# Kernel optimization log

Measured on AMD Instinct MI355X. Metric: run time of the kernel, lower is better.

The kernel has to match this reference:

```python
import jax, jax.numpy as jnp
import numpy as np

# Repo globals / config
VOCAB_SIZE = 14
TOK_DIM = 8
POS_DIM = 8
D_MODEL = TOK_DIM + POS_DIM  # 16
MAX_SEQ_LEN = 2048
N_HEADS = 2
HEAD_DIM = 3
ATTN_DIM = N_HEADS * HEAD_DIM  # 6
FFN_DIM = 3
B, T = 16, 2048
EPS = 1e-5


def _ln(x, w, b):
    m = jnp.mean(x, axis=-1, keepdims=True)
    v = jnp.var(x, axis=-1, keepdims=True)
    return (x - m) * jax.lax.rsqrt(v + EPS) * w + b


def setup_inputs() -> dict:
    key = jax.random.key(0)
    ks = jax.random.split(key, 20)
    g = lambda k, shape: (jax.random.normal(k, shape, jnp.float32) * 0.1)
    return {
        "idx": jax.random.randint(ks[0], (B, T), 0, VOCAB_SIZE),
        "tok_emb": g(ks[1], (VOCAB_SIZE, TOK_DIM)),
        "pos_enc": g(ks[2], (MAX_SEQ_LEN, POS_DIM)),
        "Wq": g(ks[3], (ATTN_DIM, POS_DIM)),
        "Wk": g(ks[4], (ATTN_DIM, POS_DIM)),
        "Wv": g(ks[5], (ATTN_DIM, TOK_DIM)),
        "Wo": g(ks[6], (D_MODEL, ATTN_DIM)),
        "ln1_w": jnp.ones((D_MODEL,), jnp.float32),
        "ln1_b": jnp.zeros((D_MODEL,), jnp.float32),
        "ln2_w": jnp.ones((D_MODEL,), jnp.float32),
        "ln2_b": jnp.zeros((D_MODEL,), jnp.float32),
        "lnf_w": jnp.ones((D_MODEL,), jnp.float32),
        "lnf_b": jnp.zeros((D_MODEL,), jnp.float32),
        "W1": g(ks[7], (FFN_DIM, D_MODEL)),
        "b1": jnp.zeros((FFN_DIM,), jnp.float32),
        "W2": g(ks[8], (D_MODEL, FFN_DIM)),
        "b2": jnp.zeros((D_MODEL,), jnp.float32),
        "Wh": g(ks[9], (TOK_DIM, D_MODEL)),
    }


def reference(idx, tok_emb, pos_enc, Wq, Wk, Wv, Wo,
              ln1_w, ln1_b, ln2_w, ln2_b, lnf_w, lnf_b,
              W1, b1, W2, b2, Wh):
    Bq, Tq = idx.shape
    tok = tok_emb[idx]                                  # [B,T,TOK_DIM]
    pos = jnp.broadcast_to(pos_enc[:Tq][None], (Bq, Tq, POS_DIM))
    x = jnp.concatenate([tok, pos], axis=-1)            # [B,T,D_MODEL]
    h = _ln(x, ln1_w, ln1_b)
    x_tok = h[..., :TOK_DIM]
    x_pos = h[..., TOK_DIM:]
    # projections (torch Linear: y = x @ W.T)
    q = (x_pos @ Wq.T).reshape(Bq, Tq, N_HEADS, HEAD_DIM).transpose(0, 2, 1, 3)
    k = (x_pos @ Wk.T).reshape(Bq, Tq, N_HEADS, HEAD_DIM).transpose(0, 2, 1, 3)
    v = (x_tok @ Wv.T).reshape(Bq, Tq, N_HEADS, HEAD_DIM).transpose(0, 2, 1, 3)
    scores = jnp.einsum('bhqd,bhkd->bhqk', q, k) / jnp.sqrt(jnp.float32(HEAD_DIM))
    mask = jnp.tril(jnp.ones((Tq, Tq), dtype=bool))
    scores = jnp.where(mask[None, None], scores, -jnp.inf)
    attn = jax.nn.softmax(scores, axis=-1)
    out = jnp.einsum('bhqk,bhkd->bhqd', attn, v)
    out = out.transpose(0, 2, 1, 3).reshape(Bq, Tq, ATTN_DIM)
    x = x + out @ Wo.T
    h2 = _ln(x, ln2_w, ln2_b)
    x = x + (jax.nn.gelu(h2 @ W1.T + b1, approximate=False) @ W2.T + b2)
    x = _ln(x, lnf_w, lnf_b)
    return (x @ Wh.T) @ tok_emb.T                       # tied head -> [B,T,VOCAB]
```

## Files before the change

kernel.cpp:

```cpp
#include <hip/hip_runtime.h>
#include <hip/hip_fp16.h>
#include <math.h>

#define BB    16
#define TT    2048
#define VOCAB 14
#define TOKD  8
#define POSD  8
#define DM    16
#define NH    2
#define HD    3
#define AD    6
#define FFND  3

#define NTOK  (BB*TT)
#define BH    (BB*NH)
#define TPB   36
#define NTILE (BH*TPB)

struct P {
    const int*   idx;
    const float* tok_emb;
    const float* pos_enc;
    const float* Wq;
    const float* Wk;
    const float* Wv;
    const float* Wo;
    const float* ln1w;
    const float* ln1b;
    const float* ln2w;
    const float* ln2b;
    const float* lnfw;
    const float* lnfb;
    const float* W1;
    const float* b1;
    const float* W2;
    const float* b2;
    const float* Wh;
    float*       out;
    float4*      qbuf;
    uint4*       kvh;
    float4*      pbuf;
};

__global__ __launch_bounds__(256) void prep_kernel(P p) {
    int gid = blockIdx.x * 256 + threadIdx.x;
    if (gid >= NTOK) return;
    int t = gid & (TT - 1);
    int b = gid >> 11;

    float x[DM];
    int tok = p.idx[gid];
    #pragma unroll
    for (int j = 0; j < TOKD; ++j) x[j]        = p.tok_emb[tok * TOKD + j];
    #pragma unroll
    for (int j = 0; j < POSD; ++j) x[TOKD + j] = p.pos_enc[t * POSD + j];

    float m = 0.f;
    #pragma unroll
    for (int j = 0; j < DM; ++j) m += x[j];
    m *= (1.f / DM);
    float v = 0.f;
    #pragma unroll
    for (int j = 0; j < DM; ++j) { float d = x[j] - m; v += d * d; }
    v *= (1.f / DM);
    float rs = rsqrtf(v + 1e-5f);
    float h[DM];
    #pragma unroll
    for (int j = 0; j < DM; ++j)
        h[j] = (x[j] - m) * rs * p.ln1w[j] + p.ln1b[j];

    float q[AD], k[AD], vv[AD];
    #pragma unroll
    for (int a = 0; a < AD; ++a) {
        float sq = 0.f, sk = 0.f, sv = 0.f;
        #pragma unroll
        for (int j = 0; j < 8; ++j) {
            sq = fmaf(p.Wq[a * 8 + j], h[TOKD + j], sq);
            sk = fmaf(p.Wk[a * 8 + j], h[TOKD + j], sk);
            sv = fmaf(p.Wv[a * 8 + j], h[j], sv);
        }
        q[a] = sq; k[a] = sk; vv[a] = sv;
    }

    const float QS = 1.4426950408889634f / 1.7320508075688772f;
    #pragma unroll
    for (int hh = 0; hh < NH; ++hh) {
        size_t base = (size_t)(b * NH + hh) * TT + t;
        p.qbuf[base] = make_float4(q[hh*3] * QS, q[hh*3+1] * QS, q[hh*3+2] * QS, 0.f);
        __half2 h0 = __floats2half2_rn(k[hh*3],    k[hh*3+1]);
        __half2 h1 = __floats2half2_rn(k[hh*3+2],  vv[hh*3]);
        __half2 h2 = __floats2half2_rn(vv[hh*3+1], vv[hh*3+2]);
        uint4 rec;
        rec.x = *reinterpret_cast<unsigned int*>(&h0);
        rec.y = *reinterpret_cast<unsigned int*>(&h1);
        rec.z = *reinterpret_cast<unsigned int*>(&h2);
        rec.w = 0u;
        p.kvh[base] = rec;
    }
}

#define UNPACK_REC(rec)                                                        \
    float2 f0 = __half22float2(*reinterpret_cast<const __half2*>(&rec.x));     \
    float2 f1 = __half22float2(*reinterpret_cast<const __half2*>(&rec.y));     \
    float2 f2 = __half22float2(*reinterpret_cast<const __half2*>(&rec.z));     \
    float k0 = f0.x, k1 = f0.y, k2 = f1.x;                                     \
    float v0 = f1.y, v1 = f2.x, v2 = f2.y;

__global__ __launch_bounds__(256) void attn_kernel(P p) {
    __shared__ uint4  skv[256];
    __shared__ float4 sq[256];
    __shared__ float4 spart[1024];

    const int tid  = threadIdx.x;
    int tile = blockIdx.x;
    int bh   = tile / TPB;
    int r    = tile - bh * TPB;
    int s    = 0;
    while (((s + 1) * (s + 2)) / 2 <= r) ++s;
    int c    = r - (s * (s + 1)) / 2;

    skv[tid] = p.kvh [(size_t)bh * TT + (c << 8) + tid];
    sq [tid] = p.qbuf[(size_t)bh * TT + (s << 8) + tid];
    __syncthreads();

    int wv   = tid >> 6;
    int lane = tid & 63;
    int kw   = wv << 6;

    float4 qr[4];
    #pragma unroll
    for (int j = 0; j < 4; ++j) qr[j] = sq[(j << 6) + lane];

    float ac[4][4];
    #pragma unroll
    for (int j = 0; j < 4; ++j)
        ac[j][0] = ac[j][1] = ac[j][2] = ac[j][3] = 0.f;

    if (c < s) {
        #pragma unroll 4
        for (int it = 0; it < 64; ++it) {
            uint4 rec = skv[kw + it];
            UNPACK_REC(rec)
            #pragma unroll
            for (int j = 0; j < 4; ++j) {
                float sc = fmaf(qr[j].x, k0, fmaf(qr[j].y, k1, qr[j].z * k2));
                float pr = __builtin_amdgcn_exp2f(sc);
                ac[j][0] = fmaf(pr, v0, ac[j][0]);
                ac[j][1] = fmaf(pr, v1, ac[j][1]);
                ac[j][2] = fmaf(pr, v2, ac[j][2]);
                ac[j][3] += pr;
            }
        }
    } else {
        #pragma unroll
        for (int j = 0; j < 4; ++j) {
            if (j < wv) continue;
            if (j == wv) {
                #pragma unroll 4
                for (int it = 0; it < 64; ++it) {
                    uint4 rec = skv[kw + it];
                    UNPACK_REC(rec)
                    float sc = fmaf(qr[j].x, k0, fmaf(qr[j].y, k1, qr[j].z * k2));
                    float pr = __builtin_amdgcn_exp2f(sc);
                    pr = (it <= lane) ? pr : 0.f;
                    ac[j][0] = fmaf(pr, v0, ac[j][0]);
                    ac[j][1] = fmaf(pr, v1, ac[j][1]);
                    ac[j][2] = fmaf(pr, v2, ac[j][2]);
                    ac[j][3] += pr;
                }
            } else {
                #pragma unroll 4
                for (int it = 0; it < 64; ++it) {
                    uint4 rec = skv[kw + it];
                    UNPACK_REC(rec)
                    float sc = fmaf(qr[j].x, k0, fmaf(qr[j].y, k1, qr[j].z * k2));
                    float pr = __builtin_amdgcn_exp2f(sc);
                    ac[j][0] = fmaf(pr, v0, ac[j][0]);
                    ac[j][1] = fmaf(pr, v1, ac[j][1]);
                    ac[j][2] = fmaf(pr, v2, ac[j][2]);
                    ac[j][3] += pr;
                }
            }
        }
    }

    #pragma unroll
    for (int j = 0; j < 4; ++j)
        spart[(wv << 8) + (j << 6) + lane] =
            make_float4(ac[j][0], ac[j][1], ac[j][2], ac[j][3]);
    __syncthreads();

    float4 p0 = spart[tid];
    float4 p1 = spart[256 + tid];
    float4 p2 = spart[512 + tid];
    float4 p3 = spart[768 + tid];
    float4 acc = make_float4(p0.x+p1.x+p2.x+p3.x, p0.y+p1.y+p2.y+p3.y,
                             p0.z+p1.z+p2.z+p3.z, p0.w+p1.w+p2.w+p3.w);
    p.pbuf[((size_t)bh * 8 + c) * TT + (s << 8) + tid] = acc;
}

__global__ __launch_bounds__(256) void epi_kernel(P p) {
    int gid = blockIdx.x * 256 + threadIdx.x;
    if (gid >= NTOK) return;
    int t = gid & (TT - 1);
    int b = gid >> 11;
    int s = t >> 8;

    float x[DM];
    int tok = p.idx[gid];
    #pragma unroll
    for (int j = 0; j < TOKD; ++j) x[j]        = p.tok_emb[tok * TOKD + j];
    #pragma unroll
    for (int j = 0; j < POSD; ++j) x[TOKD + j] = p.pos_enc[t * POSD + j];

    float att[AD];
    #pragma unroll
    for (int hh = 0; hh < NH; ++hh) {
        const float4* pp = p.pbuf + ((size_t)(b * NH + hh) * 8) * TT + t;
        float4 acc = pp[0];
        for (int c = 1; c <= s; ++c) {
            float4 e = pp[(size_t)c * TT];
            acc.x += e.x; acc.y += e.y; acc.z += e.z; acc.w += e.w;
        }
        float inv = 1.f / acc.w;
        att[hh*3+0] = acc.x * inv;
        att[hh*3+1] = acc.y * inv;
        att[hh*3+2] = acc.z * inv;
    }

    float xo[DM];
    #pragma unroll
    for (int j = 0; j < DM; ++j) {
        float sacc = x[j];
        #pragma unroll
        for (int a = 0; a < AD; ++a) sacc = fmaf(p.Wo[j * AD + a], att[a], sacc);
        xo[j] = sacc;
    }

    float m = 0.f;
    #pragma unroll
    for (int j = 0; j < DM; ++j) m += xo[j];
    m *= (1.f / DM);
    float v = 0.f;
    #pragma unroll
    for (int j = 0; j < DM; ++j) { float d = xo[j] - m; v += d * d; }
    v *= (1.f / DM);
    float rs = rsqrtf(v + 1e-5f);
    float h2[DM];
    #pragma unroll
    for (int j = 0; j < DM; ++j)
        h2[j] = (xo[j] - m) * rs * p.ln2w[j] + p.ln2b[j];

    float g[FFND];
    #pragma unroll
    for (int cc = 0; cc < FFND; ++cc) {
        float f = p.b1[cc];
        #pragma unroll
        for (int j = 0; j < DM; ++j) f = fmaf(p.W1[cc * DM + j], h2[j], f);
        g[cc] = 0.5f * f * (1.f + erff(f * 0.70710678118654752f));
    }
    float x2[DM];
    #pragma unroll
    for (int j = 0; j < DM; ++j) {
        float sacc = xo[j] + p.b2[j];
        #pragma unroll
        for (int cc = 0; cc < FFND; ++cc) sacc = fmaf(p.W2[j * FFND + cc], g[cc], sacc);
        x2[j] = sacc;
    }

    m = 0.f;
    #pragma unroll
    for (int j = 0; j < DM; ++j) m += x2[j];
    m *= (1.f / DM);
    v = 0.f;
    #pragma unroll
    for (int j = 0; j < DM; ++j) { float d = x2[j] - m; v += d * d; }
    v *= (1.f / DM);
    rs = rsqrtf(v + 1e-5f);
    float y[DM];
    #pragma unroll
    for (int j = 0; j < DM; ++j)
        y[j] = (x2[j] - m) * rs * p.lnfw[j] + p.lnfb[j];

    float t8[TOKD];
    #pragma unroll
    for (int pp = 0; pp < TOKD; ++pp) {
        float sacc = 0.f;
        #pragma unroll
        for (int j = 0; j < DM; ++j) sacc = fmaf(p.Wh[pp * DM + j], y[j], sacc);
        t8[pp] = sacc;
    }
    float* op = p.out + (size_t)gid * VOCAB;
    #pragma unroll
    for (int vcb = 0; vcb < VOCAB; ++vcb) {
        float sacc = 0.f;
        #pragma unroll
        for (int pp = 0; pp < TOKD; ++pp)
            sacc = fmaf(t8[pp], p.tok_emb[vcb * TOKD + pp], sacc);
        op[vcb] = sacc;
    }
}

extern "C" void kernel_launch(void* const* d_in, const int* in_sizes, int n_in,
                              void* d_out, int out_size, void* d_ws, size_t ws_size,
                              hipStream_t stream) {
    P p;
    p.idx     = (const int*)d_in[0];
    p.tok_emb = (const float*)d_in[1];
    p.pos_enc = (const float*)d_in[2];
    p.Wq      = (const float*)d_in[3];
    p.Wk      = (const float*)d_in[4];
    p.Wv      = (const float*)d_in[5];
    p.Wo      = (const float*)d_in[6];
    p.ln1w    = (const float*)d_in[7];
    p.ln1b    = (const float*)d_in[8];
    p.ln2w    = (const float*)d_in[9];
    p.ln2b    = (const float*)d_in[10];
    p.lnfw    = (const float*)d_in[11];
    p.lnfb    = (const float*)d_in[12];
    p.W1      = (const float*)d_in[13];
    p.b1      = (const float*)d_in[14];
    p.W2      = (const float*)d_in[15];
    p.b2      = (const float*)d_in[16];
    p.Wh      = (const float*)d_in[17];
    p.out     = (float*)d_out;
    p.qbuf    = (float4*)d_ws;
    p.kvh     = (uint4*)((char*)d_ws + (1u << 20));
    p.pbuf    = (float4*)((char*)d_ws + (2u << 20));

    prep_kernel<<<NTOK / 256, 256, 0, stream>>>(p);
    attn_kernel<<<NTILE, 256, 0, stream>>>(p);
    epi_kernel<<<NTOK / 256, 256, 0, stream>>>(p);
}
```

Baseline: 131.1 us.

## Give each attention thread one query over all keys, store K/V in fp32

The attention kernel changes its work split. Each thread now owns one query row and loops over all 256 keys of the tile, reading K and V from shared memory as broadcasts. Before, each wave handled a 64-key slice for four queries and the partial sums were combined through a shared-memory reduction with a second barrier; that reduction and barrier are gone. K/V are now stored as fp32 float4 pairs instead of packed fp16, which removes the unpack conversions but doubles the K/V global and LDS traffic. The loop also gets longer and uneven across waves in diagonal tiles.

```diff
diff --git a/kernel.cpp b/kernel.cpp
--- a/kernel.cpp
+++ b/kernel.cpp
@@ -1,5 +1,4 @@
 #include <hip/hip_runtime.h>
-#include <hip/hip_fp16.h>
 #include <math.h>
 
 #define BB    16
@@ -39,7 +38,7 @@
     const float* Wh;
     float*       out;
     float4*      qbuf;
-    uint4*       kvh;
+    float4*      kvbuf;
     float4*      pbuf;
 };
 
@@ -88,29 +87,13 @@
     for (int hh = 0; hh < NH; ++hh) {
         size_t base = (size_t)(b * NH + hh) * TT + t;
         p.qbuf[base] = make_float4(q[hh*3] * QS, q[hh*3+1] * QS, q[hh*3+2] * QS, 0.f);
-        __half2 h0 = __floats2half2_rn(k[hh*3],    k[hh*3+1]);
-        __half2 h1 = __floats2half2_rn(k[hh*3+2],  vv[hh*3]);
-        __half2 h2 = __floats2half2_rn(vv[hh*3+1], vv[hh*3+2]);
-        uint4 rec;
-        rec.x = *reinterpret_cast<unsigned int*>(&h0);
-        rec.y = *reinterpret_cast<unsigned int*>(&h1);
-        rec.z = *reinterpret_cast<unsigned int*>(&h2);
-        rec.w = 0u;
-        p.kvh[base] = rec;
-    }
-}
-
-#define UNPACK_REC(rec)                                                        \
-    float2 f0 = __half22float2(*reinterpret_cast<const __half2*>(&rec.x));     \
-    float2 f1 = __half22float2(*reinterpret_cast<const __half2*>(&rec.y));     \
-    float2 f2 = __half22float2(*reinterpret_cast<const __half2*>(&rec.z));     \
-    float k0 = f0.x, k1 = f0.y, k2 = f1.x;                                     \
-    float v0 = f1.y, v1 = f2.x, v2 = f2.y;
+        p.kvbuf[base * 2]     = make_float4(k[hh*3],  k[hh*3+1],  k[hh*3+2],  0.f);
+        p.kvbuf[base * 2 + 1] = make_float4(vv[hh*3], vv[hh*3+1], vv[hh*3+2], 0.f);
+    }
+}
 
 __global__ __launch_bounds__(256) void attn_kernel(P p) {
-    __shared__ uint4  skv[256];
-    __shared__ float4 sq[256];
-    __shared__ float4 spart[1024];
+    __shared__ float4 skv[512];
 
     const int tid  = threadIdx.x;
     int tile = blockIdx.x;
@@ -120,84 +103,47 @@
     while (((s + 1) * (s + 2)) / 2 <= r) ++s;
     int c    = r - (s * (s + 1)) / 2;
 
-    skv[tid] = p.kvh [(size_t)bh * TT + (c << 8) + tid];
-    sq [tid] = p.qbuf[(size_t)bh * TT + (s << 8) + tid];
+    const float4* gkv = p.kvbuf + ((size_t)bh * TT + (c << 8)) * 2;
+    skv[tid]       = gkv[tid];
+    skv[256 + tid] = gkv[256 + tid];
+    float4 qv = p.qbuf[(size_t)bh * TT + (s << 8) + tid];
     __syncthreads();
 
-    int wv   = tid >> 6;
+    int wv = tid >> 6;
     int lane = tid & 63;
-    int kw   = wv << 6;
-
-    float4 qr[4];
-    #pragma unroll
-    for (int j = 0; j < 4; ++j) qr[j] = sq[(j << 6) + lane];
-
-    float ac[4][4];
-    #pragma unroll
-    for (int j = 0; j < 4; ++j)
-        ac[j][0] = ac[j][1] = ac[j][2] = ac[j][3] = 0.f;
-
-    if (c < s) {
-        #pragma unroll 4
-        for (int it = 0; it < 64; ++it) {
-            uint4 rec = skv[kw + it];
-            UNPACK_REC(rec)
-            #pragma unroll
-            for (int j = 0; j < 4; ++j) {
-                float sc = fmaf(qr[j].x, k0, fmaf(qr[j].y, k1, qr[j].z * k2));
-                float pr = __builtin_amdgcn_exp2f(sc);
-                ac[j][0] = fmaf(pr, v0, ac[j][0]);
-                ac[j][1] = fmaf(pr, v1, ac[j][1]);
-                ac[j][2] = fmaf(pr, v2, ac[j][2]);
-                ac[j][3] += pr;
-            }
+    int kw = wv << 6;
+
+    float a0 = 0.f, a1 = 0.f, a2 = 0.f, l = 0.f;
+
+    int nun = (c < s) ? 256 : kw;
+    #pragma unroll 8
+    for (int it = 0; it < nun; ++it) {
+        float4 kk = skv[2 * it];
+        float4 vz = skv[2 * it + 1];
+        float sc = fmaf(qv.x, kk.x, fmaf(qv.y, kk.y, qv.z * kk.z));
+        float pr = __builtin_amdgcn_exp2f(sc);
+        a0 = fmaf(pr, vz.x, a0);
+        a1 = fmaf(pr, vz.y, a1);
+        a2 = fmaf(pr, vz.z, a2);
+        l += pr;
+    }
+    if (c == s) {
+        #pragma unroll 8
+        for (int j = 0; j < 64; ++j) {
+            float4 kk = skv[2 * (kw + j)];
+            float4 vz = skv[2 * (kw + j) + 1];
+            float sc = fmaf(qv.x, kk.x, fmaf(qv.y, kk.y, qv.z * kk.z));
+            float pr = __builtin_amdgcn_exp2f(sc);
+            pr = (j <= lane) ? pr : 0.f;
+            a0 = fmaf(pr, vz.x, a0);
+            a1 = fmaf(pr, vz.y, a1);
+            a2 = fmaf(pr, vz.z, a2);
+            l += pr;
         }
-    } else {
-        #pragma unroll
-        for (int j = 0; j < 4; ++j) {
-            if (j < wv) continue;
-            if (j == wv) {
-                #pragma unroll 4
-                for (int it = 0; it < 64; ++it) {
-                    uint4 rec = skv[kw + it];
-                    UNPACK_REC(rec)
-                    float sc = fmaf(qr[j].x, k0, fmaf(qr[j].y, k1, qr[j].z * k2));
-                    float pr = __builtin_amdgcn_exp2f(sc);
-                    pr = (it <= lane) ? pr : 0.f;
-                    ac[j][0] = fmaf(pr, v0, ac[j][0]);
-                    ac[j][1] = fmaf(pr, v1, ac[j][1]);
-                    ac[j][2] = fmaf(pr, v2, ac[j][2]);
-                    ac[j][3] += pr;
-                }
-            } else {
-                #pragma unroll 4
-                for (int it = 0; it < 64; ++it) {
-                    uint4 rec = skv[kw + it];
-                    UNPACK_REC(rec)
-                    float sc = fmaf(qr[j].x, k0, fmaf(qr[j].y, k1, qr[j].z * k2));
-                    float pr = __builtin_amdgcn_exp2f(sc);
-                    ac[j][0] = fmaf(pr, v0, ac[j][0]);
-                    ac[j][1] = fmaf(pr, v1, ac[j][1]);
-                    ac[j][2] = fmaf(pr, v2, ac[j][2]);
-                    ac[j][3] += pr;
-                }
-            }
-        }
-    }
-
-    #pragma unroll
-    for (int j = 0; j < 4; ++j)
-        spart[(wv << 8) + (j << 6) + lane] =
-            make_float4(ac[j][0], ac[j][1], ac[j][2], ac[j][3]);
-    __syncthreads();
-
-    float4 p0 = spart[tid];
-    float4 p1 = spart[256 + tid];
-    float4 p2 = spart[512 + tid];
-    float4 p3 = spart[768 + tid];
-    float4 acc = make_float4(p0.x+p1.x+p2.x+p3.x, p0.y+p1.y+p2.y+p3.y,
-                             p0.z+p1.z+p2.z+p3.z, p0.w+p1.w+p2.w+p3.w);
-    p.pbuf[((size_t)bh * 8 + c) * TT + (s << 8) + tid] = acc;
+    }
+
+    p.pbuf[((size_t)bh * 8 + c) * TT + (s << 8) + tid] =
+        make_float4(a0, a1, a2, l);
 }
 
 __global__ __launch_bounds__(256) void epi_kernel(P p) {
@@ -326,8 +272,8 @@
     p.Wh      = (const float*)d_in[17];
     p.out     = (float*)d_out;
     p.qbuf    = (float4*)d_ws;
-    p.kvh     = (uint4*)((char*)d_ws + (1u << 20));
-    p.pbuf    = (float4*)((char*)d_ws + (2u << 20));
+    p.kvbuf   = (float4*)((char*)d_ws + (1u << 20));
+    p.pbuf    = (float4*)((char*)d_ws + (3u << 20));
 
     prep_kernel<<<NTOK / 256, 256, 0, stream>>>(p);
     attn_kernel<<<NTILE, 256, 0, stream>>>(p);
```

After: 142.9 us. +9.0%, slower.
